# Performance work log

Measured on AMD Instinct MI355X. Metric: run time of the kernel, lower is better.

## Reference

```python
import jax, jax.numpy as jnp
import numpy as np

BS, T, DZ, DA, K, H = 256, 100, 32, 32, 3, 128
R_INIT, Q_INIT = 1e-3, 1e-3


def _lstm_layer(x, W_ih, W_hh, b_ih, b_hh):
    # x: [T, bs, in] -> [T, bs, H]; PyTorch gate order i, f, g, o
    bs = x.shape[1]
    h_dim = W_hh.shape[1]

    def step(carry, xt):
        h, c = carry
        g = xt @ W_ih.T + h @ W_hh.T + (b_ih + b_hh)
        i, f, gg, o = jnp.split(g, 4, axis=-1)
        c = jax.nn.sigmoid(f) * c + jax.nn.sigmoid(i) * jnp.tanh(gg)
        h = jax.nn.sigmoid(o) * jnp.tanh(c)
        return (h, c), h

    init = (jnp.zeros((bs, h_dim), x.dtype), jnp.zeros((bs, h_dim), x.dtype))
    _, hs = jax.lax.scan(step, init, x)
    return hs


def setup_inputs() -> dict:
    key = jax.random.key(0)
    ks = jax.random.split(key, 12)
    a = jax.random.normal(ks[0], (BS, T, DA), dtype=jnp.float32)
    a0 = jnp.zeros((DA,), dtype=jnp.float32)
    # A init: init_weight_A=1 gives exactly eye; add tiny noise so the K mixture
    # components are distinct (keeps the math path identical, filter stable).
    A = jnp.eye(DZ, dtype=jnp.float32)[None] + 0.05 * jax.random.normal(ks[1], (K, DZ, DZ), dtype=jnp.float32)
    # C init: init_weight_C=0 -> pure randn (scaled mildly for conditioning)
    C = 0.3 * jax.random.normal(ks[2], (K, DA, DZ), dtype=jnp.float32)
    s = 1.0 / np.sqrt(H)
    W_ih0 = s * jax.random.normal(ks[3], (4 * H, DA), dtype=jnp.float32)
    W_hh0 = s * jax.random.normal(ks[4], (4 * H, H), dtype=jnp.float32)
    b_ih0 = jnp.zeros((4 * H,), dtype=jnp.float32)
    b_hh0 = jnp.zeros((4 * H,), dtype=jnp.float32)
    W_ih1 = s * jax.random.normal(ks[5], (4 * H, H), dtype=jnp.float32)
    W_hh1 = s * jax.random.normal(ks[6], (4 * H, H), dtype=jnp.float32)
    b_ih1 = jnp.zeros((4 * H,), dtype=jnp.float32)
    b_hh1 = jnp.zeros((4 * H,), dtype=jnp.float32)
    W_lin = s * jax.random.normal(ks[7], (K, H), dtype=jnp.float32)
    b_lin = jnp.zeros((K,), dtype=jnp.float32)
    return dict(a=a, a0=a0, A=A, C=C,
                W_ih0=W_ih0, W_hh0=W_hh0, b_ih0=b_ih0, b_hh0=b_hh0,
                W_ih1=W_ih1, W_hh1=W_hh1, b_ih1=b_ih1, b_hh1=b_hh1,
                W_lin=W_lin, b_lin=b_lin)


def reference(a, a0, A, C, W_ih0, W_hh0, b_ih0, b_hh0,
              W_ih1, W_hh1, b_ih1, b_hh1, W_lin, b_lin):
    bs, seq_len, da = a.shape
    dz = A.shape[-1]
    R = R_INIT * jnp.eye(da, dtype=a.dtype)
    Q = Q_INIT * jnp.eye(dz, dtype=a.dtype)
    I = jnp.eye(dz, dtype=a.dtype)

    # Dynamics network: alpha from [a_0, a_1..a_{T-1}]
    code_and_obs = jnp.concatenate(
        [jnp.broadcast_to(a0, (bs, 1, da)), a[:, :-1, :]], axis=1)  # [bs, T, da]
    x = code_and_obs.transpose(1, 0, 2)  # [T, bs, da]
    x = _lstm_layer(x, W_ih0, W_hh0, b_ih0, b_hh0)
    x = _lstm_layer(x, W_ih1, W_hh1, b_ih1, b_hh1)
    alpha = jax.nn.softmax(x @ W_lin.T + b_lin, axis=-1)  # [T, bs, K]

    # Mixture matrices, time-major: [T, bs, dz, dz] / [T, bs, da, dz]
    A_t = jnp.einsum('tbk,kij->tbij', alpha, A)
    C_t = jnp.einsum('tbk,kij->tbij', alpha, C)
    # A used at step t is A[:, t+1]; last-step transition carry is discarded
    A_next = jnp.concatenate([A_t[1:], A_t[-1:]], axis=0)

    mu0 = jnp.zeros((bs, dz), dtype=a.dtype)
    sigma0 = jnp.broadcast_to(I, (bs, dz, dz))
    a_tm = a.transpose(1, 0, 2)  # [T, bs, da]

    def kf_step(carry, inputs):
        mu_pred, sigma_pred = carry
        at, Ct, An = inputs
        a_pred = jnp.einsum('bij,bj->bi', Ct, mu_pred)
        r = at - a_pred
        CtT = Ct.transpose(0, 2, 1)
        S = Ct @ sigma_pred @ CtT + R
        S_inv = jnp.linalg.inv(S)
        Kg = sigma_pred @ CtT @ S_inv
        mu = mu_pred + jnp.einsum('bij,bj->bi', Kg, r)
        sigma = (I - Kg @ Ct) @ sigma_pred
        sigma = 0.5 * (sigma + sigma.transpose(0, 2, 1))
        mu_p = jnp.einsum('bij,bj->bi', An, mu)
        sigma_p = An @ sigma @ An.transpose(0, 2, 1) + Q
        sigma_p = 0.5 * (sigma_p + sigma_p.transpose(0, 2, 1))
        return (mu_p, sigma_p), (mu, sigma, mu_pred, sigma_pred)

    (_, _), (means, covs, next_means, next_covs) = jax.lax.scan(
        kf_step, (mu0, sigma0), (a_tm, C_t, A_next))

    alpha_bl = alpha.transpose(1, 0, 2)
    A_bl = A_t.transpose(1, 0, 2, 3)
    C_bl = C_t.transpose(1, 0, 2, 3)
    return (means[-1], covs[-1], means, covs, next_means, next_covs,
            A_bl, C_bl, alpha_bl)
```

## Files before the change

### kernel.cpp

```cpp
#include <hip/hip_runtime.h>

static constexpr int TT = 100;
static constexpr int NB = 256;

static constexpr size_t O_ML = 0;
static constexpr size_t O_CL = 8192;
static constexpr size_t O_ME = 270336;
static constexpr size_t O_CO = 1089536;
static constexpr size_t O_NM = 27303936;
static constexpr size_t O_NC = 28123136;
static constexpr size_t O_AB = 54337536;
static constexpr size_t O_CB = 80551936;
static constexpr size_t O_AL = 106766336;

static constexpr int WS_WT0 = 0;
static constexpr int WS_WT1 = 81920;
static constexpr int WS_B0  = 212992;
static constexpr int WS_B1  = 213504;

__global__ __launch_bounds__(256) void pack_kernel(
    const float* __restrict__ Wih0, const float* __restrict__ Whh0,
    const float* __restrict__ bih0, const float* __restrict__ bhh0,
    const float* __restrict__ Wih1, const float* __restrict__ Whh1,
    const float* __restrict__ bih1, const float* __restrict__ bhh1,
    float* __restrict__ ws)
{
  int idx = blockIdx.x * 256 + threadIdx.x;
  if (idx < 81920) {
    int kb = idx >> 11, rem = idx & 2047;
    int j = rem >> 2, c = rem & 3;
    int k = kb * 4 + c;
    ws[WS_WT0 + idx] = (k < 32) ? Wih0[j * 32 + k] : Whh0[j * 128 + (k - 32)];
  } else if (idx < 212992) {
    int d = idx - 81920;
    int kb = d >> 11, rem = d & 2047;
    int j = rem >> 2, c = rem & 3;
    int k = kb * 4 + c;
    ws[WS_WT1 + d] = (k < 128) ? Wih1[j * 128 + k] : Whh1[j * 128 + (k - 128)];
  } else if (idx < 213504) {
    int j = idx - 212992;
    ws[WS_B0 + j] = bih0[j] + bhh0[j];
  } else if (idx < 214016) {
    int j = idx - 213504;
    ws[WS_B1 + j] = bih1[j] + bhh1[j];
  }
}

__device__ __forceinline__ float sigf(float x) { return 1.0f / (1.0f + expf(-x)); }
__device__ __forceinline__ float dot4(float4 w, float4 x, float acc) {
  acc = fmaf(w.x, x.x, acc); acc = fmaf(w.y, x.y, acc);
  acc = fmaf(w.z, x.z, acc); acc = fmaf(w.w, x.w, acc);
  return acc;
}

__global__ __launch_bounds__(512) void lstm_kernel(
    const float* __restrict__ a, const float* __restrict__ a0,
    const float* __restrict__ ws,
    const float* __restrict__ Wlin, const float* __restrict__ blin,
    float* __restrict__ alpha_out)
{
  __shared__ __align__(16) float xh0[2][160];
  __shared__ __align__(16) float xh1[2][256];
  __shared__ float c0s[2][128], c1s[2][128];
  __shared__ float g0[2][512], g1[2][512];
  __shared__ float bs0[512], bs1[512];
  __shared__ float wlin_s[384], blin_s[3];
  __shared__ float red[2][3][16], lgt[2][3];

  const float4* WT0 = (const float4*)(ws + WS_WT0);
  const float4* WT1 = (const float4*)(ws + WS_WT1);
  const int tid = threadIdx.x;
  const int wg = blockIdx.x;

  bs0[tid] = ws[WS_B0 + tid];
  bs1[tid] = ws[WS_B1 + tid];
  if (tid < 384) wlin_s[tid] = Wlin[tid];
  if (tid < 3) blin_s[tid] = blin[tid];
  if (tid < 128) {
#pragma unroll
    for (int bb = 0; bb < 2; ++bb) {
      xh0[bb][32 + tid] = 0.0f;
      xh1[bb][tid] = 0.0f;
      xh1[bb][128 + tid] = 0.0f;
      c0s[bb][tid] = 0.0f;
      c1s[bb][tid] = 0.0f;
    }
  }
  __syncthreads();

  for (int t = 0; t < TT; ++t) {
    if (tid < 64) {
      int bb = tid >> 5, k = tid & 31;
      xh0[bb][k] = (t == 0) ? a0[k]
                            : a[((size_t)(2 * wg + bb) * TT + (t - 1)) * 32 + k];
    }
    __syncthreads();
    {
      float acc0 = bs0[tid], acc1 = acc0;
#pragma unroll 8
      for (int kb = 0; kb < 40; ++kb) {
        float4 w = WT0[kb * 512 + tid];
        float4 x0 = *(const float4*)&xh0[0][kb * 4];
        float4 x1 = *(const float4*)&xh0[1][kb * 4];
        acc0 = dot4(w, x0, acc0);
        acc1 = dot4(w, x1, acc1);
      }
      g0[0][tid] = acc0;
      g0[1][tid] = acc1;
    }
    __syncthreads();
    if (tid < 256) {
      int bb = tid >> 7, u = tid & 127;
      float ig = sigf(g0[bb][u]);
      float fg = sigf(g0[bb][128 + u]);
      float gg = tanhf(g0[bb][256 + u]);
      float og = sigf(g0[bb][384 + u]);
      float c = fmaf(fg, c0s[bb][u], ig * gg);
      float h = og * tanhf(c);
      c0s[bb][u] = c;
      xh0[bb][32 + u] = h;
      xh1[bb][u] = h;
    }
    __syncthreads();
    {
      float acc0 = bs1[tid], acc1 = acc0;
#pragma unroll 8
      for (int kb = 0; kb < 64; ++kb) {
        float4 w = WT1[kb * 512 + tid];
        float4 x0 = *(const float4*)&xh1[0][kb * 4];
        float4 x1 = *(const float4*)&xh1[1][kb * 4];
        acc0 = dot4(w, x0, acc0);
        acc1 = dot4(w, x1, acc1);
      }
      g1[0][tid] = acc0;
      g1[1][tid] = acc1;
    }
    __syncthreads();
    if (tid < 256) {
      int bb = tid >> 7, u = tid & 127;
      float ig = sigf(g1[bb][u]);
      float fg = sigf(g1[bb][128 + u]);
      float gg = tanhf(g1[bb][256 + u]);
      float og = sigf(g1[bb][384 + u]);
      float c = fmaf(fg, c1s[bb][u], ig * gg);
      float h = og * tanhf(c);
      c1s[bb][u] = c;
      xh1[bb][128 + u] = h;
    }
    __syncthreads();
    if (tid < 96) {
      int bb = tid / 48, rr = tid % 48;
      int k = rr >> 4, l = rr & 15;
      float p = 0.0f;
#pragma unroll
      for (int c = 0; c < 8; ++c)
        p = fmaf(wlin_s[k * 128 + l * 8 + c], xh1[bb][128 + l * 8 + c], p);
      red[bb][k][l] = p;
    }
    __syncthreads();
    if (tid < 6) {
      int bb = tid / 3, k = tid % 3;
      float s = blin_s[k];
#pragma unroll
      for (int l = 0; l < 16; ++l) s += red[bb][k][l];
      lgt[bb][k] = s;
    }
    __syncthreads();
    if (tid < 2) {
      float l0 = lgt[tid][0], l1 = lgt[tid][1], l2 = lgt[tid][2];
      float mx = fmaxf(l0, fmaxf(l1, l2));
      float e0 = expf(l0 - mx), e1 = expf(l1 - mx), e2 = expf(l2 - mx);
      float inv = 1.0f / (e0 + e1 + e2);
      size_t base = ((size_t)(2 * wg + tid) * TT + t) * 3;
      alpha_out[base + 0] = e0 * inv;
      alpha_out[base + 1] = e1 * inv;
      alpha_out[base + 2] = e2 * inv;
    }
    __syncthreads();
  }
}

__device__ __forceinline__ float rl(float x, int lane) {
  return __uint_as_float(
      (unsigned)__builtin_amdgcn_readlane((int)__float_as_uint(x), lane));
}

__global__ __launch_bounds__(256) void kf_kernel(
    const float* __restrict__ a, const float* __restrict__ Ag,
    const float* __restrict__ Cg, const float* __restrict__ alpha,
    float* __restrict__ out)
{
  __shared__ float As[3][1024], Cs[3][1024];
  __shared__ float An[32][33], Ct[32][33], Sp[32][33], Mm[32][33];
  __shared__ float Ss[32][33], Tm[32][33], Xx[32][33];
  __shared__ float mu_s[32], mup_s[32], al_s[3], aln_s[3];

  const int tid = threadIdx.x;
  const int b = blockIdx.x;

  for (int q = tid; q < 3072; q += 256) {
    (&As[0][0])[q] = Ag[q];
    (&Cs[0][0])[q] = Cg[q];
  }
#pragma unroll
  for (int q = 0; q < 4; ++q) {
    int e = tid + 256 * q, i = e >> 5, j = e & 31;
    Sp[i][j] = (i == j) ? 1.0f : 0.0f;
  }
  if (tid < 32) { mu_s[tid] = 0.0f; mup_s[tid] = 0.0f; }
  __syncthreads();

  float* means_g  = out + O_ME;
  float* covs_g   = out + O_CO;
  float* nmeans_g = out + O_NM;
  float* ncovs_g  = out + O_NC;
  float* Abl_g    = out + O_AB;
  float* Cbl_g    = out + O_CB;

  for (int t = 0; t < TT; ++t) {
    if (tid < 3) {
      al_s[tid] = alpha[((size_t)b * TT + t) * 3 + tid];
    } else if (tid < 6) {
      int tn = (t < TT - 1) ? t + 1 : TT - 1;
      aln_s[tid - 3] = alpha[((size_t)b * TT + tn) * 3 + (tid - 3)];
    }
    __syncthreads();
#pragma unroll
    for (int q = 0; q < 4; ++q) {
      int e = tid + 256 * q, i = e >> 5, j = e & 31;
      float aa = al_s[0]*As[0][e] + al_s[1]*As[1][e] + al_s[2]*As[2][e];
      float an = aln_s[0]*As[0][e] + aln_s[1]*As[1][e] + aln_s[2]*As[2][e];
      float cc = al_s[0]*Cs[0][e] + al_s[1]*Cs[1][e] + al_s[2]*Cs[2][e];
      An[i][j] = an;
      Ct[i][j] = cc;
      Abl_g[((size_t)b * TT + t) * 1024 + e] = aa;
      Cbl_g[((size_t)b * TT + t) * 1024 + e] = cc;
    }
    __syncthreads();
    if (t > 0) {
#pragma unroll
      for (int q = 0; q < 4; ++q) {
        int e = tid + 256 * q, i = e >> 5, j = e & 31;
        float acc = 0.0f;
#pragma unroll
        for (int k = 0; k < 32; ++k) acc = fmaf(An[i][k], Sp[k][j], acc);
        Tm[i][j] = acc;
      }
      __syncthreads();
#pragma unroll
      for (int q = 0; q < 4; ++q) {
        int e = tid + 256 * q, i = e >> 5, j = e & 31;
        float acc = 0.0f;
#pragma unroll
        for (int k = 0; k < 32; ++k) acc = fmaf(Tm[i][k], An[j][k], acc);
        Ss[i][j] = acc;
      }
      __syncthreads();
#pragma unroll
      for (int q = 0; q < 4; ++q) {
        int e = tid + 256 * q, i = e >> 5, j = e & 31;
        float v = 0.5f * (Ss[i][j] + Ss[j][i]);
        if (i == j) v += 1.0e-3f;
        Sp[i][j] = v;
      }
      if (tid < 32) {
        float acc = 0.0f;
#pragma unroll
        for (int k = 0; k < 32; ++k) acc = fmaf(An[tid][k], mu_s[k], acc);
        mup_s[tid] = acc;
      }
      __syncthreads();
    }
#pragma unroll
    for (int q = 0; q < 4; ++q) {
      int e = tid + 256 * q, i = e >> 5, j = e & 31;
      ncovs_g[((size_t)t * NB + b) * 1024 + e] = Sp[i][j];
    }
    if (tid < 32) nmeans_g[((size_t)t * NB + b) * 32 + tid] = mup_s[tid];
#pragma unroll
    for (int q = 0; q < 4; ++q) {
      int e = tid + 256 * q, i = e >> 5, j = e & 31;
      float acc = 0.0f;
#pragma unroll
      for (int k = 0; k < 32; ++k) acc = fmaf(Ct[i][k], Sp[k][j], acc);
      Mm[i][j] = acc;
    }
    __syncthreads();
#pragma unroll
    for (int q = 0; q < 4; ++q) {
      int e = tid + 256 * q, i = e >> 5, j = e & 31;
      float acc = (i == j) ? 1.0e-3f : 0.0f;
#pragma unroll
      for (int k = 0; k < 32; ++k) acc = fmaf(Mm[i][k], Ct[j][k], acc);
      Ss[i][j] = acc;
    }
    __syncthreads();
    if (tid < 32) {
      const int l = tid;
      float s[32], m[32], rinv[32];
#pragma unroll
      for (int k = 0; k < 32; ++k) { s[k] = Ss[l][k]; m[k] = Mm[k][l]; }
      float rv = a[((size_t)b * TT + t) * 32 + l];
#pragma unroll
      for (int k = 0; k < 32; ++k) rv = fmaf(-Ct[l][k], mup_s[k], rv);
#pragma unroll
      for (int jj = 0; jj < 32; ++jj) {
        float sjj = rl(s[jj], jj);
        float ri = 1.0f / sqrtf(sjj);
        rinv[jj] = ri;
        float xj = s[jj] * ri;
        s[jj] = xj;
#pragma unroll
        for (int k = jj + 1; k < 32; ++k)
          s[k] = fmaf(-xj, rl(xj, k), s[k]);
      }
#pragma unroll
      for (int ii = 0; ii < 32; ++ii) {
        m[ii] *= rinv[ii];
        float yi = m[ii];
#pragma unroll
        for (int k = ii + 1; k < 32; ++k)
          m[k] = fmaf(-rl(s[ii], k), yi, m[k]);
      }
#pragma unroll
      for (int ii = 31; ii >= 0; --ii) {
        m[ii] *= rinv[ii];
        float xi = m[ii];
#pragma unroll
        for (int k = 0; k < ii; ++k)
          m[k] = fmaf(-rl(s[k], ii), xi, m[k]);
      }
#pragma unroll
      for (int k = 0; k < 32; ++k) Xx[k][l] = m[k];
      float mu = mup_s[l];
#pragma unroll
      for (int k = 0; k < 32; ++k) mu = fmaf(m[k], rl(rv, k), mu);
      mu_s[l] = mu;
      means_g[((size_t)t * NB + b) * 32 + l] = mu;
      if (t == TT - 1) out[O_ML + (size_t)b * 32 + l] = mu;
    }
    __syncthreads();
#pragma unroll
    for (int q = 0; q < 4; ++q) {
      int e = tid + 256 * q, i = e >> 5, j = e & 31;
      float acc = Sp[i][j];
#pragma unroll
      for (int k = 0; k < 32; ++k) acc = fmaf(-Mm[k][i], Xx[k][j], acc);
      Tm[i][j] = acc;
    }
    __syncthreads();
#pragma unroll
    for (int q = 0; q < 4; ++q) {
      int e = tid + 256 * q, i = e >> 5, j = e & 31;
      float v = 0.5f * (Tm[i][j] + Tm[j][i]);
      Sp[i][j] = v;
      covs_g[((size_t)t * NB + b) * 1024 + e] = v;
      if (t == TT - 1) out[O_CL + (size_t)b * 1024 + e] = v;
    }
    __syncthreads();
  }
}

extern "C" void kernel_launch(void* const* d_in, const int* in_sizes, int n_in,
                              void* d_out, int out_size, void* d_ws, size_t ws_size,
                              hipStream_t stream) {
  const float* a    = (const float*)d_in[0];
  const float* a0   = (const float*)d_in[1];
  const float* Ag   = (const float*)d_in[2];
  const float* Cg   = (const float*)d_in[3];
  const float* Wih0 = (const float*)d_in[4];
  const float* Whh0 = (const float*)d_in[5];
  const float* bih0 = (const float*)d_in[6];
  const float* bhh0 = (const float*)d_in[7];
  const float* Wih1 = (const float*)d_in[8];
  const float* Whh1 = (const float*)d_in[9];
  const float* bih1 = (const float*)d_in[10];
  const float* bhh1 = (const float*)d_in[11];
  const float* Wlin = (const float*)d_in[12];
  const float* blin = (const float*)d_in[13];
  float* out = (float*)d_out;
  float* ws = (float*)d_ws;

  pack_kernel<<<836, 256, 0, stream>>>(Wih0, Whh0, bih0, bhh0,
                                       Wih1, Whh1, bih1, bhh1, ws);
  lstm_kernel<<<128, 512, 0, stream>>>(a, a0, ws, Wlin, blin, out + O_AL);
  kf_kernel<<<256, 256, 0, stream>>>(a, Ag, Cg, out + O_AL, out);
}
```

Before: 3.056 ms.

## Restructure Kalman filter kernel into single-wavefront blocks with register-tiled matmuls

The Kalman filter kernel now runs one 64-lane wavefront per batch element instead of 256 threads. Each lane computes a 2x8 register tile of every 32x32 matmul using float4 LDS loads, with transposed copies of A and C kept so the second product of each pair is read row-wise. The Cholesky factorisation, forward solve and residual solve are fused into one pass: lanes 0-31 solve for the gain rows and lanes 32-63 solve the residual. The covariance update uses the symmetric L^-1 G form, which drops the explicit back-substitution and the final symmetrisation. With a single wave per block, block-wide barriers become cheap, but each block has less parallelism to hide latency and the results may round slightly differently.

```diff
diff --git a/kernel.cpp b/kernel.cpp
--- a/kernel.cpp
+++ b/kernel.cpp
@@ -180,182 +180,291 @@
   }
 }
 
-__device__ __forceinline__ float rl(float x, int lane) {
+__device__ __forceinline__ float rlf(float x, int lane) {
   return __uint_as_float(
       (unsigned)__builtin_amdgcn_readlane((int)__float_as_uint(x), lane));
 }
 
-__global__ __launch_bounds__(256) void kf_kernel(
+template <int SB>
+__device__ __forceinline__ void mmAB(const float* A, const float* B,
+                                     int i0, int j0, float (&acc)[2][8]) {
+#pragma unroll
+  for (int r = 0; r < 2; ++r)
+#pragma unroll
+    for (int c = 0; c < 8; ++c) acc[r][c] = 0.0f;
+#pragma unroll 2
+  for (int kq = 0; kq < 8; ++kq) {
+    float a0v[4], a1v[4];
+    *(float4*)a0v = *(const float4*)(A + (i0 + 0) * 36 + 4 * kq);
+    *(float4*)a1v = *(const float4*)(A + (i0 + 1) * 36 + 4 * kq);
+#pragma unroll
+    for (int kk = 0; kk < 4; ++kk) {
+      const float* Bp = B + (4 * kq + kk) * SB + j0;
+      float4 b0 = *(const float4*)Bp;
+      float4 b1 = *(const float4*)(Bp + 4);
+      acc[0][0] = fmaf(a0v[kk], b0.x, acc[0][0]);
+      acc[0][1] = fmaf(a0v[kk], b0.y, acc[0][1]);
+      acc[0][2] = fmaf(a0v[kk], b0.z, acc[0][2]);
+      acc[0][3] = fmaf(a0v[kk], b0.w, acc[0][3]);
+      acc[0][4] = fmaf(a0v[kk], b1.x, acc[0][4]);
+      acc[0][5] = fmaf(a0v[kk], b1.y, acc[0][5]);
+      acc[0][6] = fmaf(a0v[kk], b1.z, acc[0][6]);
+      acc[0][7] = fmaf(a0v[kk], b1.w, acc[0][7]);
+      acc[1][0] = fmaf(a1v[kk], b0.x, acc[1][0]);
+      acc[1][1] = fmaf(a1v[kk], b0.y, acc[1][1]);
+      acc[1][2] = fmaf(a1v[kk], b0.z, acc[1][2]);
+      acc[1][3] = fmaf(a1v[kk], b0.w, acc[1][3]);
+      acc[1][4] = fmaf(a1v[kk], b1.x, acc[1][4]);
+      acc[1][5] = fmaf(a1v[kk], b1.y, acc[1][5]);
+      acc[1][6] = fmaf(a1v[kk], b1.z, acc[1][6]);
+      acc[1][7] = fmaf(a1v[kk], b1.w, acc[1][7]);
+    }
+  }
+}
+
+__device__ __forceinline__ void stBlock(float* M, int i0, int j0,
+                                        const float (&acc)[2][8]) {
+#pragma unroll
+  for (int r = 0; r < 2; ++r) {
+    float4 v0 = make_float4(acc[r][0], acc[r][1], acc[r][2], acc[r][3]);
+    float4 v1 = make_float4(acc[r][4], acc[r][5], acc[r][6], acc[r][7]);
+    *(float4*)(M + (i0 + r) * 36 + j0) = v0;
+    *(float4*)(M + (i0 + r) * 36 + j0 + 4) = v1;
+  }
+}
+
+__global__ __launch_bounds__(64, 1) void kf_kernel(
     const float* __restrict__ a, const float* __restrict__ Ag,
-    const float* __restrict__ Cg, const float* __restrict__ alpha,
-    float* __restrict__ out)
+    const float* __restrict__ Cg, const float* alpha, float* out)
 {
-  __shared__ float As[3][1024], Cs[3][1024];
-  __shared__ float An[32][33], Ct[32][33], Sp[32][33], Mm[32][33];
-  __shared__ float Ss[32][33], Tm[32][33], Xx[32][33];
-  __shared__ float mu_s[32], mup_s[32], al_s[3], aln_s[3];
-
-  const int tid = threadIdx.x;
+  __shared__ __align__(16) float As[3072], Cs[3072];
+  __shared__ __align__(16) float An[32 * 36], Ct[32 * 36], Sp[32 * 36];
+  __shared__ __align__(16) float TM[32 * 36], Ss[32 * 36], Gt[32 * 36];
+  __shared__ __align__(16) float AnT[1024], CtT[1024], Gc[1024];
+  __shared__ float muv[32], mupv[32], rv[32];
+
+  const int l = threadIdx.x;
   const int b = blockIdx.x;
-
-  for (int q = tid; q < 3072; q += 256) {
-    (&As[0][0])[q] = Ag[q];
-    (&Cs[0][0])[q] = Cg[q];
-  }
-#pragma unroll
-  for (int q = 0; q < 4; ++q) {
-    int e = tid + 256 * q, i = e >> 5, j = e & 31;
-    Sp[i][j] = (i == j) ? 1.0f : 0.0f;
-  }
-  if (tid < 32) { mu_s[tid] = 0.0f; mup_s[tid] = 0.0f; }
+  const int i0 = 2 * (l >> 2), j0 = 8 * (l & 3);
+
+  const float4* Ag4 = (const float4*)Ag;
+  const float4* Cg4 = (const float4*)Cg;
+  float4* As4 = (float4*)As;
+  float4* Cs4 = (float4*)Cs;
+#pragma unroll
+  for (int q = 0; q < 12; ++q) {
+    As4[l + 64 * q] = Ag4[l + 64 * q];
+    Cs4[l + 64 * q] = Cg4[l + 64 * q];
+  }
+#pragma unroll
+  for (int r = 0; r < 2; ++r)
+#pragma unroll
+    for (int c = 0; c < 8; ++c)
+      Sp[(i0 + r) * 36 + j0 + c] = (i0 + r == j0 + c) ? 1.0f : 0.0f;
+  if (l < 32) { muv[l] = 0.0f; mupv[l] = 0.0f; }
   __syncthreads();
 
-  float* means_g  = out + O_ME;
-  float* covs_g   = out + O_CO;
-  float* nmeans_g = out + O_NM;
-  float* ncovs_g  = out + O_NC;
-  float* Abl_g    = out + O_AB;
-  float* Cbl_g    = out + O_CB;
+  float* mg  = out + O_ME;
+  float* cg  = out + O_CO;
+  float* nmg = out + O_NM;
+  float* ncg = out + O_NC;
+  float* abg = out + O_AB;
+  float* cbg = out + O_CB;
 
   for (int t = 0; t < TT; ++t) {
-    if (tid < 3) {
-      al_s[tid] = alpha[((size_t)b * TT + t) * 3 + tid];
-    } else if (tid < 6) {
-      int tn = (t < TT - 1) ? t + 1 : TT - 1;
-      aln_s[tid - 3] = alpha[((size_t)b * TT + tn) * 3 + (tid - 3)];
-    }
-    __syncthreads();
-#pragma unroll
-    for (int q = 0; q < 4; ++q) {
-      int e = tid + 256 * q, i = e >> 5, j = e & 31;
-      float aa = al_s[0]*As[0][e] + al_s[1]*As[1][e] + al_s[2]*As[2][e];
-      float an = aln_s[0]*As[0][e] + aln_s[1]*As[1][e] + aln_s[2]*As[2][e];
-      float cc = al_s[0]*Cs[0][e] + al_s[1]*Cs[1][e] + al_s[2]*Cs[2][e];
-      An[i][j] = an;
-      Ct[i][j] = cc;
-      Abl_g[((size_t)b * TT + t) * 1024 + e] = aa;
-      Cbl_g[((size_t)b * TT + t) * 1024 + e] = cc;
-    }
-    __syncthreads();
+    float al0 = alpha[((size_t)b * TT + t) * 3 + 0];
+    float al1 = alpha[((size_t)b * TT + t) * 3 + 1];
+    float al2 = alpha[((size_t)b * TT + t) * 3 + 2];
+    {
+      float4* Abl4 = (float4*)(abg + ((size_t)b * TT + t) * 1024);
+      float4* Cbl4 = (float4*)(cbg + ((size_t)b * TT + t) * 1024);
+#pragma unroll
+      for (int q = 0; q < 4; ++q) {
+        int f = l + 64 * q;
+        int i = f >> 3, j4 = (f & 7) * 4;
+        float4 x0 = As4[f], x1 = As4[256 + f], x2 = As4[512 + f];
+        float4 av;
+        av.x = al0 * x0.x + al1 * x1.x + al2 * x2.x;
+        av.y = al0 * x0.y + al1 * x1.y + al2 * x2.y;
+        av.z = al0 * x0.z + al1 * x1.z + al2 * x2.z;
+        av.w = al0 * x0.w + al1 * x1.w + al2 * x2.w;
+        float4 y0 = Cs4[f], y1 = Cs4[256 + f], y2 = Cs4[512 + f];
+        float4 cv;
+        cv.x = al0 * y0.x + al1 * y1.x + al2 * y2.x;
+        cv.y = al0 * y0.y + al1 * y1.y + al2 * y2.y;
+        cv.z = al0 * y0.z + al1 * y1.z + al2 * y2.z;
+        cv.w = al0 * y0.w + al1 * y1.w + al2 * y2.w;
+        *(float4*)&An[i * 36 + j4] = av;
+        *(float4*)&Ct[i * 36 + j4] = cv;
+        AnT[(j4 + 0) * 32 + i] = av.x;
+        AnT[(j4 + 1) * 32 + i] = av.y;
+        AnT[(j4 + 2) * 32 + i] = av.z;
+        AnT[(j4 + 3) * 32 + i] = av.w;
+        CtT[(j4 + 0) * 32 + i] = cv.x;
+        CtT[(j4 + 1) * 32 + i] = cv.y;
+        CtT[(j4 + 2) * 32 + i] = cv.z;
+        CtT[(j4 + 3) * 32 + i] = cv.w;
+        Abl4[f] = av;
+        Cbl4[f] = cv;
+      }
+    }
+    __syncthreads();
+
     if (t > 0) {
-#pragma unroll
-      for (int q = 0; q < 4; ++q) {
-        int e = tid + 256 * q, i = e >> 5, j = e & 31;
-        float acc = 0.0f;
-#pragma unroll
-        for (int k = 0; k < 32; ++k) acc = fmaf(An[i][k], Sp[k][j], acc);
-        Tm[i][j] = acc;
-      }
+      float acc[2][8];
+      mmAB<36>(An, Sp, i0, j0, acc);
+      stBlock(TM, i0, j0, acc);
       __syncthreads();
-#pragma unroll
-      for (int q = 0; q < 4; ++q) {
-        int e = tid + 256 * q, i = e >> 5, j = e & 31;
-        float acc = 0.0f;
-#pragma unroll
-        for (int k = 0; k < 32; ++k) acc = fmaf(Tm[i][k], An[j][k], acc);
-        Ss[i][j] = acc;
+      mmAB<32>(TM, AnT, i0, j0, acc);
+      stBlock(Ss, i0, j0, acc);
+      if (l < 32) {
+        float s = 0.0f;
+#pragma unroll
+        for (int kq = 0; kq < 8; ++kq) {
+          float4 avv = *(const float4*)&An[l * 36 + 4 * kq];
+          float4 mv = *(const float4*)&muv[4 * kq];
+          s += avv.x * mv.x + avv.y * mv.y + avv.z * mv.z + avv.w * mv.w;
+        }
+        mupv[l] = s;
       }
       __syncthreads();
 #pragma unroll
-      for (int q = 0; q < 4; ++q) {
-        int e = tid + 256 * q, i = e >> 5, j = e & 31;
-        float v = 0.5f * (Ss[i][j] + Ss[j][i]);
-        if (i == j) v += 1.0e-3f;
-        Sp[i][j] = v;
-      }
-      if (tid < 32) {
-        float acc = 0.0f;
-#pragma unroll
-        for (int k = 0; k < 32; ++k) acc = fmaf(An[tid][k], mu_s[k], acc);
-        mup_s[tid] = acc;
-      }
+      for (int r = 0; r < 2; ++r)
+#pragma unroll
+        for (int c = 0; c < 8; ++c) {
+          float x = Ss[(i0 + r) * 36 + j0 + c];
+          float xt = Ss[(j0 + c) * 36 + i0 + r];
+          float v = 0.5f * (x + xt) + ((i0 + r == j0 + c) ? 1.0e-3f : 0.0f);
+          Sp[(i0 + r) * 36 + j0 + c] = v;
+        }
       __syncthreads();
     }
-#pragma unroll
-    for (int q = 0; q < 4; ++q) {
-      int e = tid + 256 * q, i = e >> 5, j = e & 31;
-      ncovs_g[((size_t)t * NB + b) * 1024 + e] = Sp[i][j];
-    }
-    if (tid < 32) nmeans_g[((size_t)t * NB + b) * 32 + tid] = mup_s[tid];
-#pragma unroll
-    for (int q = 0; q < 4; ++q) {
-      int e = tid + 256 * q, i = e >> 5, j = e & 31;
-      float acc = 0.0f;
-#pragma unroll
-      for (int k = 0; k < 32; ++k) acc = fmaf(Ct[i][k], Sp[k][j], acc);
-      Mm[i][j] = acc;
-    }
-    __syncthreads();
-#pragma unroll
-    for (int q = 0; q < 4; ++q) {
-      int e = tid + 256 * q, i = e >> 5, j = e & 31;
-      float acc = (i == j) ? 1.0e-3f : 0.0f;
-#pragma unroll
-      for (int k = 0; k < 32; ++k) acc = fmaf(Mm[i][k], Ct[j][k], acc);
-      Ss[i][j] = acc;
-    }
-    __syncthreads();
-    if (tid < 32) {
-      const int l = tid;
-      float s[32], m[32], rinv[32];
-#pragma unroll
-      for (int k = 0; k < 32; ++k) { s[k] = Ss[l][k]; m[k] = Mm[k][l]; }
-      float rv = a[((size_t)b * TT + t) * 32 + l];
-#pragma unroll
-      for (int k = 0; k < 32; ++k) rv = fmaf(-Ct[l][k], mup_s[k], rv);
-#pragma unroll
-      for (int jj = 0; jj < 32; ++jj) {
-        float sjj = rl(s[jj], jj);
-        float ri = 1.0f / sqrtf(sjj);
-        rinv[jj] = ri;
-        float xj = s[jj] * ri;
-        s[jj] = xj;
-#pragma unroll
-        for (int k = jj + 1; k < 32; ++k)
-          s[k] = fmaf(-xj, rl(xj, k), s[k]);
-      }
-#pragma unroll
-      for (int ii = 0; ii < 32; ++ii) {
-        m[ii] *= rinv[ii];
-        float yi = m[ii];
-#pragma unroll
-        for (int k = ii + 1; k < 32; ++k)
-          m[k] = fmaf(-rl(s[ii], k), yi, m[k]);
-      }
-#pragma unroll
-      for (int ii = 31; ii >= 0; --ii) {
-        m[ii] *= rinv[ii];
-        float xi = m[ii];
-#pragma unroll
-        for (int k = 0; k < ii; ++k)
-          m[k] = fmaf(-rl(s[k], ii), xi, m[k]);
-      }
-#pragma unroll
-      for (int k = 0; k < 32; ++k) Xx[k][l] = m[k];
-      float mu = mup_s[l];
-#pragma unroll
-      for (int k = 0; k < 32; ++k) mu = fmaf(m[k], rl(rv, k), mu);
-      mu_s[l] = mu;
-      means_g[((size_t)t * NB + b) * 32 + l] = mu;
-      if (t == TT - 1) out[O_ML + (size_t)b * 32 + l] = mu;
-    }
-    __syncthreads();
-#pragma unroll
-    for (int q = 0; q < 4; ++q) {
-      int e = tid + 256 * q, i = e >> 5, j = e & 31;
-      float acc = Sp[i][j];
-#pragma unroll
-      for (int k = 0; k < 32; ++k) acc = fmaf(-Mm[k][i], Xx[k][j], acc);
-      Tm[i][j] = acc;
-    }
-    __syncthreads();
-#pragma unroll
-    for (int q = 0; q < 4; ++q) {
-      int e = tid + 256 * q, i = e >> 5, j = e & 31;
-      float v = 0.5f * (Tm[i][j] + Tm[j][i]);
-      Sp[i][j] = v;
-      covs_g[((size_t)t * NB + b) * 1024 + e] = v;
-      if (t == TT - 1) out[O_CL + (size_t)b * 1024 + e] = v;
+
+    {
+      float4* dst = (float4*)(ncg + ((size_t)t * NB + b) * 1024);
+#pragma unroll
+      for (int r = 0; r < 2; ++r) {
+        float4 v0 = *(const float4*)&Sp[(i0 + r) * 36 + j0];
+        float4 v1 = *(const float4*)&Sp[(i0 + r) * 36 + j0 + 4];
+        dst[((i0 + r) * 32 + j0) >> 2] = v0;
+        dst[(((i0 + r) * 32 + j0) >> 2) + 1] = v1;
+      }
+      if (l < 32) nmg[((size_t)t * NB + b) * 32 + l] = mupv[l];
+    }
+
+    {
+      float acc[2][8];
+      mmAB<36>(Ct, Sp, i0, j0, acc);
+      stBlock(TM, i0, j0, acc);
+#pragma unroll
+      for (int r = 0; r < 2; ++r)
+#pragma unroll
+        for (int c = 0; c < 8; ++c)
+          Gt[(j0 + c) * 36 + i0 + r] = acc[r][c];
+      __syncthreads();
+      mmAB<32>(TM, CtT, i0, j0, acc);
+#pragma unroll
+      for (int r = 0; r < 2; ++r)
+#pragma unroll
+        for (int c = 0; c < 8; ++c)
+          if (i0 + r == j0 + c) acc[r][c] += 1.0e-3f;
+      stBlock(Ss, i0, j0, acc);
+    }
+    if (l < 32) {
+      float rvv = a[((size_t)b * TT + t) * 32 + l];
+#pragma unroll
+      for (int kq = 0; kq < 8; ++kq) {
+        float4 cvv = *(const float4*)&Ct[l * 36 + 4 * kq];
+        float4 mv = *(const float4*)&mupv[4 * kq];
+        rvv -= cvv.x * mv.x + cvv.y * mv.y + cvv.z * mv.z + cvv.w * mv.w;
+      }
+      rv[l] = rvv;
+    }
+    __syncthreads();
+
+    float s[32], m[32];
+    {
+      const float* srow = Ss + (l & 31) * 36;
+#pragma unroll
+      for (int kq = 0; kq < 8; ++kq) {
+        float4 v = *(const float4*)(srow + 4 * kq);
+        s[4 * kq + 0] = v.x; s[4 * kq + 1] = v.y;
+        s[4 * kq + 2] = v.z; s[4 * kq + 3] = v.w;
+      }
+      if (l < 32) {
+        const float* mrow = Gt + l * 36;
+#pragma unroll
+        for (int kq = 0; kq < 8; ++kq) {
+          float4 v = *(const float4*)(mrow + 4 * kq);
+          m[4 * kq + 0] = v.x; m[4 * kq + 1] = v.y;
+          m[4 * kq + 2] = v.z; m[4 * kq + 3] = v.w;
+        }
+      } else {
+#pragma unroll
+        for (int kq = 0; kq < 8; ++kq) {
+          float4 v = *(const float4*)&rv[4 * kq];
+          m[4 * kq + 0] = v.x; m[4 * kq + 1] = v.y;
+          m[4 * kq + 2] = v.z; m[4 * kq + 3] = v.w;
+        }
+      }
+    }
+#pragma unroll
+    for (int jj = 0; jj < 32; ++jj) {
+      float sjj = rlf(s[jj], jj);
+      float ri = 1.0f / sqrtf(sjj);
+      float xj = s[jj] * ri;
+      s[jj] = xj;
+      m[jj] *= ri;
+#pragma unroll
+      for (int k = jj + 1; k < 32; ++k) {
+        float lkj = rlf(xj, k);
+        s[k] = fmaf(-xj, lkj, s[k]);
+        m[k] = fmaf(-lkj, m[jj], m[k]);
+      }
+    }
+    if (l < 32) {
+#pragma unroll
+      for (int kq = 0; kq < 8; ++kq) {
+        float4 v = make_float4(m[4 * kq + 0], m[4 * kq + 1],
+                               m[4 * kq + 2], m[4 * kq + 3]);
+        *(float4*)&Gt[l * 36 + 4 * kq] = v;
+      }
+#pragma unroll
+      for (int k = 0; k < 32; ++k) Gc[k * 32 + l] = m[k];
+    }
+    {
+      float mu = mupv[l & 31];
+#pragma unroll
+      for (int k = 0; k < 32; ++k) mu = fmaf(m[k], rlf(m[k], 32), mu);
+      if (l < 32) {
+        muv[l] = mu;
+        mg[((size_t)t * NB + b) * 32 + l] = mu;
+        if (t == TT - 1) out[O_ML + (size_t)b * 32 + l] = mu;
+      }
+    }
+    __syncthreads();
+
+    {
+      float acc[2][8];
+      mmAB<32>(Gt, Gc, i0, j0, acc);
+      float4* dst = (float4*)(cg + ((size_t)t * NB + b) * 1024);
+      float4* dstL = (float4*)(out + O_CL + (size_t)b * 1024);
+#pragma unroll
+      for (int r = 0; r < 2; ++r) {
+        float vv[8];
+#pragma unroll
+        for (int c = 0; c < 8; ++c) {
+          float v = Sp[(i0 + r) * 36 + j0 + c] - acc[r][c];
+          Sp[(i0 + r) * 36 + j0 + c] = v;
+          vv[c] = v;
+        }
+        float4 v0 = make_float4(vv[0], vv[1], vv[2], vv[3]);
+        float4 v1 = make_float4(vv[4], vv[5], vv[6], vv[7]);
+        int fi = ((i0 + r) * 32 + j0) >> 2;
+        dst[fi] = v0;
+        dst[fi + 1] = v1;
+        if (t == TT - 1) { dstL[fi] = v0; dstL[fi + 1] = v1; }
+      }
     }
     __syncthreads();
   }
@@ -384,5 +493,5 @@
   pack_kernel<<<836, 256, 0, stream>>>(Wih0, Whh0, bih0, bhh0,
                                        Wih1, Whh1, bih1, bhh1, ws);
   lstm_kernel<<<128, 512, 0, stream>>>(a, a0, ws, Wlin, blin, out + O_AL);
-  kf_kernel<<<256, 256, 0, stream>>>(a, Ag, Cg, out + O_AL, out);
-}
+  kf_kernel<<<256, 64, 0, stream>>>(a, Ag, Cg, out + O_AL, out);
+}
```

Result: faster. 2.713 ms (-11.2%).
